# Kernel tuning notes

Hardware: AMD Instinct MI355X
Metric: run time of the kernel (lower is better)

## Reference

```python
import jax, jax.numpy as jnp
import numpy as np

B, M, N = 64, 100, 100
LAMBDA_COORD = 1.0
LAMBDA_CONF = 1.0
EPS = 1e-12


def _hungarian(cost):
    """O(n^3) Hungarian algorithm (potentials / e-maxx variant) on a square
    numpy cost matrix. Returns row_to_col assignment (length n)."""
    n = cost.shape[0]
    u = np.zeros(n + 1)
    v = np.zeros(n + 1)
    p = np.zeros(n + 1, dtype=np.int64)   # p[j] = row matched to column j
    way = np.zeros(n + 1, dtype=np.int64)
    for i in range(1, n + 1):
        p[0] = i
        j0 = 0
        minv = np.full(n + 1, np.inf)
        used = np.zeros(n + 1, dtype=bool)
        while True:
            used[j0] = True
            i0 = p[j0]
            js = np.nonzero(~used)[0]
            js = js[js > 0]
            cur = cost[i0 - 1, js - 1] - u[i0] - v[js]
            upd = cur < minv[js]
            minv[js] = np.where(upd, cur, minv[js])
            way[js] = np.where(upd, j0, way[js])
            j1 = js[np.argmin(minv[js])]
            delta = minv[j1]
            uj = np.nonzero(used)[0]
            u[p[uj]] += delta
            v[uj] -= delta
            minv[js] -= delta
            j0 = j1
            if p[j0] == 0:
                break
        while j0:
            j1 = way[j0]
            p[j0] = p[j1]
            j0 = j1
    row_to_col = np.full(n, -1, dtype=np.int64)
    for j in range(1, n + 1):
        row_to_col[p[j] - 1] = j - 1
    return row_to_col


def _match(pred_xy, target_xy, target_conf):
    """Host-side matching (mirrors the original's CPU round trip).
    Returns padded rows [B,P], cols [B,P] (cols index into the ORIGINAL target
    axis) and cnt [B] = number of matched pairs (min(M, K_valid))."""
    Bb, Mm, _ = pred_xy.shape
    Nn = target_xy.shape[1]
    P = min(Mm, Nn)
    rows = np.zeros((Bb, P), np.int64)
    cols = np.zeros((Bb, P), np.int64)
    cnt = np.zeros(Bb, np.int64)
    for b in range(Bb):
        valid = np.nonzero(target_conf[b] > 0.5)[0]
        K = valid.size
        if K == 0:
            continue
        tgt = target_xy[b, valid]                       # [K,2]
        cost = np.linalg.norm(pred_xy[b][:, None, :] - tgt[None, :, :], axis=-1)  # [M,K]
        n = max(Mm, K)
        sq = np.zeros((n, n))                           # zero-pad to square
        sq[:Mm, :K] = cost
        r2c = _hungarian(sq)
        k = 0
        for r in range(Mm):
            c = r2c[r]
            if 0 <= c < K:
                rows[b, k] = r
                cols[b, k] = valid[c]
                k += 1
        cnt[b] = k
    return rows, cols, cnt


def _loss(pred, target, rows, cols, cnt):
    Bb, P = rows.shape
    bidx = jnp.arange(Bb)[:, None]
    mp = pred[bidx, rows]                                # [B,P,3] matched preds
    mt = target[bidx, cols]                              # [B,P,3] matched tgts
    mask = (jnp.arange(P)[None, :] < cnt[:, None]).astype(pred.dtype)
    denom = jnp.maximum(cnt, 1).astype(pred.dtype)
    # per-batch F.mse_loss: mean over cnt*2 coord elements
    se = (((mp[..., :2] - mt[..., :2]) ** 2).sum(-1) * mask).sum(-1)
    loss_coord = jnp.where(cnt > 0, se / (2.0 * denom), 0.0).sum()
    # per-batch F.binary_cross_entropy: mean over cnt elements
    pconf = jnp.clip(mp[..., 2], EPS, 1.0 - EPS)
    tconf = mt[..., 2]
    bce = -(tconf * jnp.log(pconf) + (1.0 - tconf) * jnp.log1p(-pconf))
    loss_conf = jnp.where(cnt > 0, (bce * mask).sum(-1) / denom, 0.0).sum()
    return (LAMBDA_COORD * loss_coord + LAMBDA_CONF * loss_conf) / Bb


def setup_inputs() -> dict:
    key = jax.random.key(0)
    k1, k2 = jax.random.split(key)
    pred = jax.random.uniform(k1, (B, M, 3), dtype=jnp.float32)
    target = jax.random.uniform(k2, (B, N, 3), dtype=jnp.float32)
    return {"pred": pred, "target": target}


def reference(pred, target):
    pred_np = np.asarray(pred)
    tgt_np = np.asarray(target)
    rows, cols, cnt = _match(pred_np[..., :2], tgt_np[..., :2], tgt_np[..., 2])
    rows = jnp.asarray(rows)
    cols = jnp.asarray(cols)
    cnt = jnp.asarray(cnt)
    return _loss(pred, target, rows, cols, cnt)
```

## Files before the change

kernel.cpp:

```cpp
#include <hip/hip_runtime.h>
#include <math.h>

#define BATCH 64
#define MM 100
#define NN 100
#define ST 101
#define BIGCLAIM 0x7fffffff
#define SENTK 0xFFFFFFFFu


__device__ __forceinline__ int readlane_i(int v, int lane) {
    return __builtin_amdgcn_readlane(v, lane);
}
__device__ __forceinline__ float readlane_f(float v, int lane) {
    return __int_as_float(__builtin_amdgcn_readlane(__float_as_int(v), lane));
}

__device__ __forceinline__ unsigned pack_key(float x, int col) {
    unsigned u = __float_as_uint(x);
    u ^= ((unsigned)((int)u >> 31)) | 0x80000000u;
    return (u & 0xFFFFFF80u) | (unsigned)col;
}
__device__ __forceinline__ float key_val(unsigned k) {
    unsigned u = k & 0xFFFFFF80u;
    u = (u & 0x80000000u) ? (u ^ 0x80000000u) : ~u;
    return __uint_as_float(u);
}

template<int CTRL>
__device__ __forceinline__ unsigned dpp_mov_u32(unsigned x) {
    return (unsigned)__builtin_amdgcn_update_dpp((int)x, (int)x, CTRL, 0xF, 0xF, false);
}
template<int CTRL>
__device__ __forceinline__ unsigned dpp_min_u32(unsigned x) {
    unsigned p = dpp_mov_u32<CTRL>(x);
    return x < p ? x : p;
}
__device__ __forceinline__ unsigned wave_min_u32(unsigned x) {
    x = dpp_min_u32<0xB1>(x);
    x = dpp_min_u32<0x4E>(x);
    x = dpp_min_u32<0x141>(x);
    x = dpp_min_u32<0x140>(x);
    x = dpp_min_u32<0x142>(x);
    x = dpp_min_u32<0x143>(x);
    return (unsigned)readlane_i((int)x, 63);
}
template<int CTRL>
__device__ __forceinline__ void min2_step(unsigned &lo, unsigned &hi) {
    unsigned olo = dpp_mov_u32<CTRL>(lo);
    unsigned ohi = dpp_mov_u32<CTRL>(hi);
    unsigned mn  = lo < olo ? lo : olo;
    unsigned mx  = lo < olo ? olo : lo;
    unsigned m2  = hi < ohi ? hi : ohi;
    lo = mn;
    hi = mx < m2 ? mx : m2;
}
__device__ __forceinline__ void wave_min2_u32(unsigned a, unsigned b,
                                              unsigned &k1, unsigned &k2) {
    unsigned lo = a < b ? a : b;
    unsigned hi = a < b ? b : a;
    min2_step<0xB1>(lo, hi);
    min2_step<0x4E>(lo, hi);
    min2_step<0x141>(lo, hi);
    min2_step<0x140>(lo, hi);
    min2_step<0x142>(lo, hi);
    min2_step<0x143>(lo, hi);
    k1 = (unsigned)readlane_i((int)lo, 63);
    k2 = (unsigned)readlane_i((int)hi, 63);
}


__global__ __launch_bounds__(128) void hung_all(
        const float* __restrict__ pred, const float* __restrict__ target,
        double* __restrict__ wsloss, unsigned* __restrict__ counter,
        float* __restrict__ out) {
    const int b    = blockIdx.x;
    const int tid  = threadIdx.x;
    const int lane = tid & 63;
    const int wave = tid >> 6;
    const float* P = pred + b * MM * 3;
    const float* T = target + b * NN * 3;

    __shared__ float px[MM], py[MM], pc[MM];
    __shared__ float tvx[NN], tvy[NN], tvc[NN];
    __shared__ float Tc[NN * ST];
    __shared__ int   rmini[NN];
    __shared__ int   claimArr[MM + 1];
    __shared__ int   Ksh;

    float pxA = P[3*lane], pyA = P[3*lane+1];
    float pxB = 0.f, pyB = 0.f;
    const bool colBvalid = (lane + 64 < MM);
    if (colBvalid) { pxB = P[3*(lane+64)]; pyB = P[3*(lane+64)+1]; }

    if (wave == 0) {
        px[lane] = pxA; py[lane] = pyA; pc[lane] = P[3*lane+2];
        if (colBvalid) { px[lane+64]=pxB; py[lane+64]=pyB; pc[lane+64]=P[3*(lane+64)+2]; }
        float cxA=T[3*lane], cyA=T[3*lane+1], ccA=T[3*lane+2];
        bool vA_ = ccA > 0.5f;
        float cxB=0.f, cyB=0.f, ccB=0.f; bool vB_=false;
        if (lane + 64 < NN) {
            cxB=T[3*(lane+64)]; cyB=T[3*(lane+64)+1]; ccB=T[3*(lane+64)+2];
            vB_ = ccB > 0.5f;
        }
        unsigned long long mAv = __ballot(vA_);
        unsigned long long mBv = __ballot(vB_);
        int nA_ = __popcll(mAv);
        int K0  = nA_ + __popcll(mBv);
        unsigned long long below = (1ull << lane) - 1ull;
        if (vA_) { int q = __popcll(mAv & below);       tvx[q]=cxA; tvy[q]=cyA; tvc[q]=ccA; }
        if (vB_) { int q = nA_ + __popcll(mBv & below); tvx[q]=cxB; tvy[q]=cyB; tvc[q]=ccB; }
        if (lane == 0) Ksh = K0;
        claimArr[lane] = BIGCLAIM;
        if (lane + 64 <= MM) claimArr[lane + 64] = BIGCLAIM;
    }
    __syncthreads();
    const int K = Ksh;

    const int jA = lane;
    const int jB = lane + 64;
    const bool validB = (jB <= MM);
    const int idxA = (jA >= 1) ? (jA - 1) : 0;
    const int idxB = validB ? (jB - 1) : (MM - 1);

    double loss = 0.0;
    if (K > 0) {
        float txA = (lane < K)      ? tvx[lane]      : 0.f;
        float tyA = (lane < K)      ? tvy[lane]      : 0.f;
        float txB = (lane + 64 < K) ? tvx[lane + 64] : 0.f;
        float tyB = (lane + 64 < K) ? tvy[lane + 64] : 0.f;

        for (int c = wave; c < K; c += 2) {
            float tx = (c < 64) ? readlane_f(txA, c) : readlane_f(txB, c - 64);
            float ty = (c < 64) ? readlane_f(tyA, c) : readlane_f(tyB, c - 64);
            float dxA = __fsub_rn(pxA, tx), dyA = __fsub_rn(pyA, ty);
            float cA = __fsqrt_rn(__fadd_rn(__fmul_rn(dxA,dxA), __fmul_rn(dyA,dyA)));
            Tc[c*ST + lane] = cA;
            unsigned kB = SENTK;
            if (colBvalid) {
                float dxB = __fsub_rn(pxB, tx), dyB = __fsub_rn(pyB, ty);
                float cB = __fsqrt_rn(__fadd_rn(__fmul_rn(dxB,dxB), __fmul_rn(dyB,dyB)));
                Tc[c*ST + lane + 64] = cB;
                kB = pack_key(cB, lane + 64);
            }
            unsigned kA = pack_key(cA, lane);
            unsigned k = wave_min_u32(kA < kB ? kA : kB);
            if (lane == 0) rmini[c] = (int)(k & 127u);
        }
        __syncthreads();
        if (wave == 1) return;

        int rA_ = lane + 1, rB_ = lane + 65;
        int argA = 0, argB = 0;
        if (lane < K)      { argA = rmini[lane] + 1;      atomicMin(&claimArr[argA], rA_); }
        if (lane + 64 < K) { argB = rmini[lane + 64] + 1; atomicMin(&claimArr[argB], rB_); }
        __threadfence_block();
        int pA = 0, pB = 0;
        if (jA >= 1) { int c0 = claimArr[jA]; pA = (c0 != BIGCLAIM) ? c0 : 0; }
        if (validB)  { int c0 = claimArr[jB]; pB = (c0 != BIGCLAIM) ? c0 : 0; }
        bool freeA = (lane < K)      && (claimArr[argA] != rA_);
        bool freeB = (lane + 64 < K) && (claimArr[argB] != rB_);
        unsigned long long fA = __ballot(freeA);
        unsigned long long fB = __ballot(freeB);

        float mcA = 0.f, mcB = 0.f;
        if (pA > 0) mcA = Tc[(pA-1)*ST + idxA];
        if (pB > 0) mcB = Tc[(pB-1)*ST + idxB];

        float vvA = 0.f, vvB = 0.f;

        unsigned long long dijA = 0ull, dijB = 0ull;
        for (int sweep = 0; sweep < 2; ++sweep) {
            unsigned long long curA = fA, curB = fB;
            fA = 0ull; fB = 0ull;
            int rr = curA ? (int)__ffsll(curA)
                          : (curB ? (int)__ffsll(curB) + 64 : 0);
            float cA = 0.f, cB = 0.f;
            if (rr) { cA = Tc[(rr-1)*ST + idxA]; cB = Tc[(rr-1)*ST + idxB]; }
            while (curA | curB) {
                int r;
                if (curA) { r = (int)__ffsll(curA);      curA &= curA - 1; }
                else      { r = (int)__ffsll(curB) + 64; curB &= curB - 1; }
                int r2 = curA ? (int)__ffsll(curA)
                              : (curB ? (int)__ffsll(curB) + 64 : r);
                float nxA = Tc[(r2-1)*ST + idxA];
                float nxB = Tc[(r2-1)*ST + idxB];

                float rcA = cA - vvA;
                float rcB = cB - vvB;
                unsigned kA = (jA >= 1) ? pack_key(rcA, jA) : SENTK;
                unsigned kB = validB ? pack_key(rcB, jB) : SENTK;
                unsigned k1, k2;
                wave_min2_u32(kA, kB, k1, k2);
                int j1 = (int)(k1 & 127u);
                float dv = fmaxf(key_val(k2) - key_val(k1), 0.f);

                int holder = (j1 < 64) ? readlane_i(pA, j1)
                                       : readlane_i(pB, j1 & 63);
                if (jA == j1)            { vvA -= dv; pA = r; mcA = cA; }
                if (validB && jB == j1)  { vvB -= dv; pB = r; mcB = cB; }
                if (holder != 0) {
                    if (sweep == 0) {
                        if (holder <= 64) fA |= 1ull << (holder - 1);
                        else              fB |= 1ull << (holder - 65);
                    } else {
                        if (holder <= 64) dijA |= 1ull << (holder - 1);
                        else              dijB |= 1ull << (holder - 65);
                    }
                }
                cA = nxA; cB = nxB;
            }
        }

        const float INF32 = __builtin_inff();
        float pcAf = 0.f, pcBf = 0.f;
        {
            int r0 = dijA ? (int)__ffsll(dijA)
                          : (dijB ? (int)__ffsll(dijB) + 64 : 0);
            if (r0) { pcAf = Tc[(r0-1)*ST + idxA]; pcBf = Tc[(r0-1)*ST + idxB]; }
        }
        while (dijA | dijB) {
            int r;
            if (dijA) { r = (int)__ffsll(dijA);      dijA &= dijA - 1; }
            else      { r = (int)__ffsll(dijB) + 64; dijB &= dijB - 1; }

            float minvA = INF32, minvB = INF32;
            int wayA = 0, wayB = 0;
            bool usedA = (lane == 0), usedB = false;
            float dpopA = 0.f, dpopB = 0.f;
            if (lane == 0) pA = r;
            int j0 = 0, jfree = -1;
            float dstar = 0.f, S = 0.f;
            float cA_f = pcAf, cB_f = pcBf;

            for (int it = 0; it <= MM; ++it) {
                if (jA >= 1 && !usedA) {
                    float t = (cA_f - vvA) + S;
                    if (t < minvA) { minvA = t; wayA = j0; }
                }
                if (validB && !usedB) {
                    float t = (cB_f - vvB) + S;
                    if (t < minvB) { minvB = t; wayB = j0; }
                }
                unsigned kA = (jA >= 1 && !usedA) ? pack_key(minvA, jA) : SENTK;
                unsigned kB = (validB && !usedB) ? pack_key(minvB, jB) : SENTK;
                unsigned k1 = wave_min_u32(kA < kB ? kA : kB);
                int j1 = (int)(k1 & 127u);
                float delta = key_val(k1);

                if (jA == j1) { usedA = true; dpopA = delta; }
                if (jB == j1) { usedB = true; dpopB = delta; }

                int pj1 = (j1 < 64) ? readlane_i(pA, j1)
                                    : readlane_i(pB, j1 & 63);
                if (pj1 == 0) { jfree = j1; dstar = delta; break; }

                float mcj = (j1 < 64) ? readlane_f(mcA, j1) : readlane_f(mcB, j1 & 63);
                float vj  = (j1 < 64) ? readlane_f(vvA, j1) : readlane_f(vvB, j1 & 63);
                cA_f = Tc[(pj1-1)*ST + idxA];
                cB_f = Tc[(pj1-1)*ST + idxB];
                S = (delta - mcj) + vj;
                j0 = j1;
            }

            {
                int r1 = dijA ? (int)__ffsll(dijA)
                              : (dijB ? (int)__ffsll(dijB) + 64 : 0);
                if (r1) { pcAf = Tc[(r1-1)*ST + idxA]; pcBf = Tc[(r1-1)*ST + idxB]; }
            }
            if (usedA && jA >= 1) vvA += dpopA - dstar;
            if (usedB)            vvB += dpopB - dstar;

            int jc = jfree;
            for (int s = 0; s <= MM && jc > 0; ++s) {
                int wa = readlane_i(wayA, jc & 63);
                int wb = readlane_i(wayB, jc & 63);
                int w  = (jc < 64) ? wa : wb;
                int pa = readlane_i(pA, w & 63);
                int pb = readlane_i(pB, w & 63);
                int pw = (w < 64) ? pa : pb;
                if (jA == jc) { pA = pw; mcA = Tc[(pw-1)*ST + idxA]; }
                if (validB && jB == jc) { pB = pw; mcB = Tc[(pw-1)*ST + idxB]; }
                jc = w;
            }
        }

        double se = 0.0, bce = 0.0;
        if (jA >= 1 && pA > 0) {
            int rr2 = jA - 1, c = pA - 1;
            float dx = __fsub_rn(px[rr2], tvx[c]);
            float dy = __fsub_rn(py[rr2], tvy[c]);
            se = (double)dx*(double)dx + (double)dy*(double)dy;
            double pcv = (double)pc[rr2];
            pcv = fmin(fmax(pcv, 1e-12), 1.0 - 1e-12);
            double tc = (double)tvc[c];
            bce = -(tc * log(pcv) + (1.0 - tc) * log1p(-pcv));
        }
        if (validB && pB > 0) {
            int rr2 = jB - 1, c = pB - 1;
            float dx = __fsub_rn(px[rr2], tvx[c]);
            float dy = __fsub_rn(py[rr2], tvy[c]);
            se += (double)dx*(double)dx + (double)dy*(double)dy;
            double pcv = (double)pc[rr2];
            pcv = fmin(fmax(pcv, 1e-12), 1.0 - 1e-12);
            double tc = (double)tvc[c];
            bce += -(tc * log(pcv) + (1.0 - tc) * log1p(-pcv));
        }
        for (int m = 1; m < 64; m <<= 1) {
            se  += __shfl_xor(se,  m, 64);
            bce += __shfl_xor(bce, m, 64);
        }
        loss = se / (2.0 * (double)K) + bce / (double)K;
    } else {
        if (wave == 1) return;
    }

    unsigned old = 0;
    if (lane == 0) {
        wsloss[b] = loss;
        __threadfence();
        old = atomicAdd(counter, 1u);
    }
    unsigned long long lastm = __ballot((lane == 0) && (old == BATCH - 1));
    if (lastm) {
        __threadfence();
        unsigned long long bits =
            atomicCAS((unsigned long long*)&wsloss[lane], 0ull, 0ull);
        double v = __longlong_as_double(bits);
        for (int m = 1; m < 64; m <<= 1) v += __shfl_xor(v, m, 64);
        if (lane == 0) out[0] = (float)(v / (double)BATCH);
    }
}

extern "C" void kernel_launch(void* const* d_in, const int* in_sizes, int n_in,
                              void* d_out, int out_size, void* d_ws, size_t ws_size,
                              hipStream_t stream) {
    const float* pred   = (const float*)d_in[0];
    const float* target = (const float*)d_in[1];
    double*   wsl = (double*)d_ws;
    unsigned* cnt = (unsigned*)((char*)d_ws + 512);
    float*    out = (float*)d_out;
    hipMemsetAsync(cnt, 0, sizeof(unsigned), stream);
    hung_all<<<dim3(BATCH), dim3(128), 0, stream>>>(pred, target, wsl, cnt, out);
}
```

Measured before the change: 56.14 us.

## Replace sequential auction sweeps with parallel bidding rounds before Dijkstra phase

Replaces the two serial per-row auction sweeps, which do one wave-wide min2 reduction per free row, with up to 12 rounds of parallel Bertsekas-style bidding. In each round every free row scans all columns itself, bids via atomicMin on a shared slot, and the winners update the shared assignment and column prices. Any rows still free go on to the existing Dijkstra augmentation. This trades serial reduction latency for per-lane 100-column scans plus extra shared-memory traffic and barriers. The number of rows left for the costly augmentation phase may also change.

```diff
diff --git a/kernel.cpp b/kernel.cpp
--- a/kernel.cpp
+++ b/kernel.cpp
@@ -44,29 +44,6 @@
     x = dpp_min_u32<0x142>(x);
     x = dpp_min_u32<0x143>(x);
     return (unsigned)readlane_i((int)x, 63);
-}
-template<int CTRL>
-__device__ __forceinline__ void min2_step(unsigned &lo, unsigned &hi) {
-    unsigned olo = dpp_mov_u32<CTRL>(lo);
-    unsigned ohi = dpp_mov_u32<CTRL>(hi);
-    unsigned mn  = lo < olo ? lo : olo;
-    unsigned mx  = lo < olo ? olo : lo;
-    unsigned m2  = hi < ohi ? hi : ohi;
-    lo = mn;
-    hi = mx < m2 ? mx : m2;
-}
-__device__ __forceinline__ void wave_min2_u32(unsigned a, unsigned b,
-                                              unsigned &k1, unsigned &k2) {
-    unsigned lo = a < b ? a : b;
-    unsigned hi = a < b ? b : a;
-    min2_step<0xB1>(lo, hi);
-    min2_step<0x4E>(lo, hi);
-    min2_step<0x141>(lo, hi);
-    min2_step<0x140>(lo, hi);
-    min2_step<0x142>(lo, hi);
-    min2_step<0x143>(lo, hi);
-    k1 = (unsigned)readlane_i((int)lo, 63);
-    k2 = (unsigned)readlane_i((int)hi, 63);
 }
 
 
@@ -86,6 +63,11 @@
     __shared__ float Tc[NN * ST];
     __shared__ int   rmini[NN];
     __shared__ int   claimArr[MM + 1];
+    __shared__ int   pArr[MM + 1];
+    __shared__ float vArr[MM + 1];
+    __shared__ int   bidSlot[MM + 1];
+    __shared__ int   rowFree[NN + 1];
+    __shared__ int   flist[NN];
     __shared__ int   Ksh;
 
     float pxA = P[3*lane], pyA = P[3*lane+1];
@@ -112,7 +94,11 @@
         if (vB_) { int q = nA_ + __popcll(mBv & below); tvx[q]=cxB; tvy[q]=cyB; tvc[q]=ccB; }
         if (lane == 0) Ksh = K0;
         claimArr[lane] = BIGCLAIM;
-        if (lane + 64 <= MM) claimArr[lane + 64] = BIGCLAIM;
+        pArr[lane] = 0; vArr[lane] = 0.f;
+        if (lane + 64 <= MM) {
+            claimArr[lane + 64] = BIGCLAIM;
+            pArr[lane + 64] = 0; vArr[lane + 64] = 0.f;
+        }
     }
     __syncthreads();
     const int K = Ksh;
@@ -150,6 +136,8 @@
         __syncthreads();
         if (wave == 1) return;
 
+        const float INF32 = __builtin_inff();
+
         int rA_ = lane + 1, rB_ = lane + 65;
         int argA = 0, argB = 0;
         if (lane < K)      { argA = rmini[lane] + 1;      atomicMin(&claimArr[argA], rA_); }
@@ -163,56 +151,73 @@
         unsigned long long fA = __ballot(freeA);
         unsigned long long fB = __ballot(freeB);
 
+        if (jA >= 1) pArr[jA] = pA;
+        if (validB)  pArr[jB] = pB;
+        rowFree[rA_] = freeA ? 1 : 0;
+        if (rB_ <= NN) rowFree[rB_] = freeB ? 1 : 0;
+        __threadfence_block();
+
+        for (int round = 0; round < 12; ++round) {
+            if (!(fA | fB)) break;
+            int F = __popcll(fA) + __popcll(fB);
+            unsigned long long below = (1ull << lane) - 1ull;
+            if ((fA >> lane) & 1ull)
+                flist[__popcll(fA & below)] = lane + 1;
+            if ((fB >> lane) & 1ull)
+                flist[__popcll(fA) + __popcll(fB & below)] = lane + 65;
+            bidSlot[lane] = BIGCLAIM;
+            if (lane + 64 <= MM) bidSlot[lane + 64] = BIGCLAIM;
+            __threadfence_block();
+
+            int nact = F < 64 ? F : 64;
+            bool active = lane < nact;
+            int r = active ? flist[lane] : 1;
+
+            float m1a = INF32, m2a = INF32, m1b = INF32, m2b = INF32;
+            int j1a = 1, j1b = 2;
+            const float* rowp = &Tc[(r - 1) * ST];
+            for (int j = 1; j <= MM; j += 2) {
+                float va = vArr[j];
+                float vb = vArr[j + 1];
+                float ca = rowp[j - 1] - va;
+                float cb = rowp[j]     - vb;
+                if (ca < m1a) { m2a = m1a; m1a = ca; j1a = j; }
+                else if (ca < m2a) { m2a = ca; }
+                if (cb < m1b) { m2b = m1b; m1b = cb; j1b = j + 1; }
+                else if (cb < m2b) { m2b = cb; }
+            }
+            float min1, second; int j1;
+            if (m1a <= m1b) { min1 = m1a; j1 = j1a; second = fminf(m2a, m1b); }
+            else            { min1 = m1b; j1 = j1b; second = fminf(m2b, m1a); }
+            float gap = fmaxf(second - min1, 0.f);
+
+            if (active) atomicMin(&bidSlot[j1], r);
+            __threadfence_block();
+
+            if (active && bidSlot[j1] == r) {
+                int h = pArr[j1];
+                pArr[j1] = r;
+                vArr[j1] = vArr[j1] - gap;
+                rowFree[r] = 0;
+                if (h) rowFree[h] = 1;
+            }
+            __threadfence_block();
+
+            fA = __ballot(rowFree[lane + 1] != 0);
+            bool bfree = (lane + 65 <= NN) && (rowFree[lane + 65] != 0);
+            fB = __ballot(bfree);
+        }
+        __threadfence_block();
+
+        pA = pArr[jA];
+        pB = validB ? pArr[jB] : 0;
+        float vvA = vArr[jA];
+        float vvB = validB ? vArr[jB] : 0.f;
         float mcA = 0.f, mcB = 0.f;
         if (pA > 0) mcA = Tc[(pA-1)*ST + idxA];
         if (pB > 0) mcB = Tc[(pB-1)*ST + idxB];
 
-        float vvA = 0.f, vvB = 0.f;
-
-        unsigned long long dijA = 0ull, dijB = 0ull;
-        for (int sweep = 0; sweep < 2; ++sweep) {
-            unsigned long long curA = fA, curB = fB;
-            fA = 0ull; fB = 0ull;
-            int rr = curA ? (int)__ffsll(curA)
-                          : (curB ? (int)__ffsll(curB) + 64 : 0);
-            float cA = 0.f, cB = 0.f;
-            if (rr) { cA = Tc[(rr-1)*ST + idxA]; cB = Tc[(rr-1)*ST + idxB]; }
-            while (curA | curB) {
-                int r;
-                if (curA) { r = (int)__ffsll(curA);      curA &= curA - 1; }
-                else      { r = (int)__ffsll(curB) + 64; curB &= curB - 1; }
-                int r2 = curA ? (int)__ffsll(curA)
-                              : (curB ? (int)__ffsll(curB) + 64 : r);
-                float nxA = Tc[(r2-1)*ST + idxA];
-                float nxB = Tc[(r2-1)*ST + idxB];
-
-                float rcA = cA - vvA;
-                float rcB = cB - vvB;
-                unsigned kA = (jA >= 1) ? pack_key(rcA, jA) : SENTK;
-                unsigned kB = validB ? pack_key(rcB, jB) : SENTK;
-                unsigned k1, k2;
-                wave_min2_u32(kA, kB, k1, k2);
-                int j1 = (int)(k1 & 127u);
-                float dv = fmaxf(key_val(k2) - key_val(k1), 0.f);
-
-                int holder = (j1 < 64) ? readlane_i(pA, j1)
-                                       : readlane_i(pB, j1 & 63);
-                if (jA == j1)            { vvA -= dv; pA = r; mcA = cA; }
-                if (validB && jB == j1)  { vvB -= dv; pB = r; mcB = cB; }
-                if (holder != 0) {
-                    if (sweep == 0) {
-                        if (holder <= 64) fA |= 1ull << (holder - 1);
-                        else              fB |= 1ull << (holder - 65);
-                    } else {
-                        if (holder <= 64) dijA |= 1ull << (holder - 1);
-                        else              dijB |= 1ull << (holder - 65);
-                    }
-                }
-                cA = nxA; cB = nxB;
-            }
-        }
-
-        const float INF32 = __builtin_inff();
+        unsigned long long dijA = fA, dijB = fB;
         float pcAf = 0.f, pcBf = 0.f;
         {
             int r0 = dijA ? (int)__ffsll(dijA)
```

Result: slower. 108.5 us (+93.3%).

## Batch two auction rows per wave reduction and use per-thread row argmin

Applied to the files above, without the earlier changes.

The initial row-argmin no longer runs a wave-wide DPP reduction for every cost row. Each thread now scans its own row of the shared cost matrix with four independent min chains. The auction sweep now handles two free rows per iteration, with one interleaved dual top-2 DPP reduction. If both rows want the same column, the second row is pushed back to the queue. This roughly halves the serialized reduction latency, at the price of more registers and extra branching. It could also change the order of auction steps.

```diff
diff --git a/kernel.cpp b/kernel.cpp
--- a/kernel.cpp
+++ b/kernel.cpp
@@ -46,27 +46,36 @@
     return (unsigned)readlane_i((int)x, 63);
 }
 template<int CTRL>
-__device__ __forceinline__ void min2_step(unsigned &lo, unsigned &hi) {
-    unsigned olo = dpp_mov_u32<CTRL>(lo);
-    unsigned ohi = dpp_mov_u32<CTRL>(hi);
-    unsigned mn  = lo < olo ? lo : olo;
-    unsigned mx  = lo < olo ? olo : lo;
-    unsigned m2  = hi < ohi ? hi : ohi;
-    lo = mn;
-    hi = mx < m2 ? mx : m2;
-}
-__device__ __forceinline__ void wave_min2_u32(unsigned a, unsigned b,
-                                              unsigned &k1, unsigned &k2) {
-    unsigned lo = a < b ? a : b;
-    unsigned hi = a < b ? b : a;
-    min2_step<0xB1>(lo, hi);
-    min2_step<0x4E>(lo, hi);
-    min2_step<0x141>(lo, hi);
-    min2_step<0x140>(lo, hi);
-    min2_step<0x142>(lo, hi);
-    min2_step<0x143>(lo, hi);
-    k1 = (unsigned)readlane_i((int)lo, 63);
-    k2 = (unsigned)readlane_i((int)hi, 63);
+__device__ __forceinline__ void min2_step2(unsigned &lo0, unsigned &hi0,
+                                           unsigned &lo1, unsigned &hi1) {
+    unsigned olo0 = dpp_mov_u32<CTRL>(lo0);
+    unsigned olo1 = dpp_mov_u32<CTRL>(lo1);
+    unsigned ohi0 = dpp_mov_u32<CTRL>(hi0);
+    unsigned ohi1 = dpp_mov_u32<CTRL>(hi1);
+    unsigned mn0 = lo0 < olo0 ? lo0 : olo0;
+    unsigned mx0 = lo0 < olo0 ? olo0 : lo0;
+    unsigned m20 = hi0 < ohi0 ? hi0 : ohi0;
+    lo0 = mn0; hi0 = mx0 < m20 ? mx0 : m20;
+    unsigned mn1 = lo1 < olo1 ? lo1 : olo1;
+    unsigned mx1 = lo1 < olo1 ? olo1 : lo1;
+    unsigned m21 = hi1 < ohi1 ? hi1 : ohi1;
+    lo1 = mn1; hi1 = mx1 < m21 ? mx1 : m21;
+}
+__device__ __forceinline__ void wave_min2x2_u32(
+        unsigned a0, unsigned b0, unsigned a1, unsigned b1,
+        unsigned &k1_0, unsigned &k2_0, unsigned &k1_1, unsigned &k2_1) {
+    unsigned lo0 = a0 < b0 ? a0 : b0, hi0 = a0 < b0 ? b0 : a0;
+    unsigned lo1 = a1 < b1 ? a1 : b1, hi1 = a1 < b1 ? b1 : a1;
+    min2_step2<0xB1>(lo0, hi0, lo1, hi1);
+    min2_step2<0x4E>(lo0, hi0, lo1, hi1);
+    min2_step2<0x141>(lo0, hi0, lo1, hi1);
+    min2_step2<0x140>(lo0, hi0, lo1, hi1);
+    min2_step2<0x142>(lo0, hi0, lo1, hi1);
+    min2_step2<0x143>(lo0, hi0, lo1, hi1);
+    k1_0 = (unsigned)readlane_i((int)lo0, 63);
+    k2_0 = (unsigned)readlane_i((int)hi0, 63);
+    k1_1 = (unsigned)readlane_i((int)lo1, 63);
+    k2_1 = (unsigned)readlane_i((int)hi1, 63);
 }
 
 
@@ -136,19 +145,35 @@
             float dxA = __fsub_rn(pxA, tx), dyA = __fsub_rn(pyA, ty);
             float cA = __fsqrt_rn(__fadd_rn(__fmul_rn(dxA,dxA), __fmul_rn(dyA,dyA)));
             Tc[c*ST + lane] = cA;
-            unsigned kB = SENTK;
             if (colBvalid) {
                 float dxB = __fsub_rn(pxB, tx), dyB = __fsub_rn(pyB, ty);
                 float cB = __fsqrt_rn(__fadd_rn(__fmul_rn(dxB,dxB), __fmul_rn(dyB,dyB)));
                 Tc[c*ST + lane + 64] = cB;
-                kB = pack_key(cB, lane + 64);
-            }
-            unsigned kA = pack_key(cA, lane);
-            unsigned k = wave_min_u32(kA < kB ? kA : kB);
-            if (lane == 0) rmini[c] = (int)(k & 127u);
+            }
+        }
+        __syncthreads();
+
+        if (tid < K) {
+            const float* rp = &Tc[tid * ST];
+            float m0=rp[0], m1=rp[1], m2=rp[2], m3=rp[3];
+            int   i0=0,    i1=1,    i2=2,    i3=3;
+            #pragma unroll
+            for (int j = 4; j < MM; j += 4) {
+                float v0=rp[j], v1=rp[j+1], v2=rp[j+2], v3=rp[j+3];
+                if (v0<m0){m0=v0;i0=j;}
+                if (v1<m1){m1=v1;i1=j+1;}
+                if (v2<m2){m2=v2;i2=j+2;}
+                if (v3<m3){m3=v3;i3=j+3;}
+            }
+            if (m1<m0){m0=m1;i0=i1;}
+            if (m3<m2){m2=m3;i2=i3;}
+            if (m2<m0){m0=m2;i0=i2;}
+            rmini[tid] = i0;
         }
         __syncthreads();
         if (wave == 1) return;
+
+        const float INF32 = __builtin_inff();
 
         int rA_ = lane + 1, rB_ = lane + 65;
         int argA = 0, argB = 0;
@@ -166,53 +191,78 @@
         float mcA = 0.f, mcB = 0.f;
         if (pA > 0) mcA = Tc[(pA-1)*ST + idxA];
         if (pB > 0) mcB = Tc[(pB-1)*ST + idxB];
-
         float vvA = 0.f, vvB = 0.f;
 
         unsigned long long dijA = 0ull, dijB = 0ull;
         for (int sweep = 0; sweep < 2; ++sweep) {
             unsigned long long curA = fA, curB = fB;
             fA = 0ull; fB = 0ull;
-            int rr = curA ? (int)__ffsll(curA)
-                          : (curB ? (int)__ffsll(curB) + 64 : 0);
-            float cA = 0.f, cB = 0.f;
-            if (rr) { cA = Tc[(rr-1)*ST + idxA]; cB = Tc[(rr-1)*ST + idxB]; }
             while (curA | curB) {
                 int r;
                 if (curA) { r = (int)__ffsll(curA);      curA &= curA - 1; }
                 else      { r = (int)__ffsll(curB) + 64; curB &= curB - 1; }
-                int r2 = curA ? (int)__ffsll(curA)
-                              : (curB ? (int)__ffsll(curB) + 64 : r);
-                float nxA = Tc[(r2-1)*ST + idxA];
-                float nxB = Tc[(r2-1)*ST + idxB];
-
-                float rcA = cA - vvA;
-                float rcB = cB - vvB;
-                unsigned kA = (jA >= 1) ? pack_key(rcA, jA) : SENTK;
-                unsigned kB = validB ? pack_key(rcB, jB) : SENTK;
-                unsigned k1, k2;
-                wave_min2_u32(kA, kB, k1, k2);
-                int j1 = (int)(k1 & 127u);
-                float dv = fmaxf(key_val(k2) - key_val(k1), 0.f);
-
-                int holder = (j1 < 64) ? readlane_i(pA, j1)
-                                       : readlane_i(pB, j1 & 63);
-                if (jA == j1)            { vvA -= dv; pA = r; mcA = cA; }
-                if (validB && jB == j1)  { vvB -= dv; pB = r; mcB = cB; }
-                if (holder != 0) {
+                int s = 0;
+                if (curA)      { s = (int)__ffsll(curA);      curA &= curA - 1; }
+                else if (curB) { s = (int)__ffsll(curB) + 64; curB &= curB - 1; }
+
+                float cAr = Tc[(r-1)*ST + idxA];
+                float cBr = Tc[(r-1)*ST + idxB];
+                float cAs = 0.f, cBs = 0.f;
+                if (s) { cAs = Tc[(s-1)*ST + idxA]; cBs = Tc[(s-1)*ST + idxB]; }
+
+                float rcAr = cAr - vvA, rcBr = cBr - vvB;
+                unsigned kAr = (jA >= 1) ? pack_key(rcAr, jA) : SENTK;
+                unsigned kBr = validB ? pack_key(rcBr, jB) : SENTK;
+                unsigned kAs = SENTK, kBs = SENTK;
+                if (s) {
+                    float rcAs = cAs - vvA, rcBs = cBs - vvB;
+                    kAs = (jA >= 1) ? pack_key(rcAs, jA) : SENTK;
+                    kBs = validB ? pack_key(rcBs, jB) : SENTK;
+                }
+                unsigned k1r, k2r, k1s, k2s;
+                wave_min2x2_u32(kAr, kBr, kAs, kBs, k1r, k2r, k1s, k2s);
+
+                int j1r = (int)(k1r & 127u);
+                float dvr = fmaxf(key_val(k2r) - key_val(k1r), 0.f);
+                int holderR = (j1r < 64) ? readlane_i(pA, j1r)
+                                         : readlane_i(pB, j1r & 63);
+                if (jA == j1r)            { vvA -= dvr; pA = r; mcA = cAr; }
+                if (validB && jB == j1r)  { vvB -= dvr; pB = r; mcB = cBr; }
+                if (holderR != 0) {
                     if (sweep == 0) {
-                        if (holder <= 64) fA |= 1ull << (holder - 1);
-                        else              fB |= 1ull << (holder - 65);
+                        if (holderR <= 64) fA |= 1ull << (holderR - 1);
+                        else               fB |= 1ull << (holderR - 65);
                     } else {
-                        if (holder <= 64) dijA |= 1ull << (holder - 1);
-                        else              dijB |= 1ull << (holder - 65);
+                        if (holderR <= 64) dijA |= 1ull << (holderR - 1);
+                        else               dijB |= 1ull << (holderR - 65);
                     }
                 }
-                cA = nxA; cB = nxB;
-            }
-        }
-
-        const float INF32 = __builtin_inff();
+
+                if (s) {
+                    int j1s = (int)(k1s & 127u);
+                    if (j1s == j1r) {
+                        if (s <= 64) curA |= 1ull << (s - 1);
+                        else         curB |= 1ull << (s - 65);
+                    } else {
+                        float dvs = fmaxf(key_val(k2s) - key_val(k1s), 0.f);
+                        int holderS = (j1s < 64) ? readlane_i(pA, j1s)
+                                                 : readlane_i(pB, j1s & 63);
+                        if (jA == j1s)            { vvA -= dvs; pA = s; mcA = cAs; }
+                        if (validB && jB == j1s)  { vvB -= dvs; pB = s; mcB = cBs; }
+                        if (holderS != 0) {
+                            if (sweep == 0) {
+                                if (holderS <= 64) fA |= 1ull << (holderS - 1);
+                                else               fB |= 1ull << (holderS - 65);
+                            } else {
+                                if (holderS <= 64) dijA |= 1ull << (holderS - 1);
+                                else               dijB |= 1ull << (holderS - 65);
+                            }
+                        }
+                    }
+                }
+            }
+        }
+
         float pcAf = 0.f, pcBf = 0.f;
         {
             int r0 = dijA ? (int)__ffsll(dijA)
@@ -272,7 +322,7 @@
             if (usedB)            vvB += dpopB - dstar;
 
             int jc = jfree;
-            for (int s = 0; s <= MM && jc > 0; ++s) {
+            for (int s2 = 0; s2 <= MM && jc > 0; ++s2) {
                 int wa = readlane_i(wayA, jc & 63);
                 int wb = readlane_i(wayB, jc & 63);
                 int w  = (jc < 64) ? wa : wb;
```

After: 56.17 us. About the same (+0.1%).
